# Performance work log

Hardware: AMD Instinct MI355X
Metric: run time of the kernel (lower is better)

Reference implementation:

```python
import jax, jax.numpy as jnp
import numpy as np

N, E, G, ND, H, C, L = 100000, 640000, 1000, 128, 128, 10, 4
ATOMS_PER_GRAPH = 100  # N = G * ATOMS_PER_GRAPH
NEG_SLOPE = 0.01  # nn.LeakyReLU default


def setup_inputs() -> dict:
    key = jax.random.key(0)
    ks = jax.random.split(key, 16)
    s = 0.05
    return {
        "node_attr": jax.random.normal(ks[0], (N, ND), jnp.float32),
        "edge_index": jax.random.randint(ks[1], (2, E), 0, N, jnp.int64),
        "num_atoms": jnp.full((G,), ATOMS_PER_GRAPH, dtype=jnp.int64),
        "enc_W": jax.random.normal(ks[2], (ND, H), jnp.float32) * s,
        "enc_b": jnp.zeros((H,), jnp.float32),
        "gcn_W": jax.random.normal(ks[3], (L, H, H), jnp.float32) * s,
        "gcn_b": jnp.zeros((L, H), jnp.float32),
        "r_W1": jax.random.normal(ks[4], (H, H), jnp.float32) * s,
        "r_b1": jnp.zeros((H,), jnp.float32),
        "r_W2": jax.random.normal(ks[5], (H, H), jnp.float32) * s,
        "r_b2": jnp.zeros((H,), jnp.float32),
        "s_W1": jax.random.normal(ks[6], (H, H), jnp.float32) * s,
        "s_b1": jnp.zeros((H,), jnp.float32),
        "s_W2": jax.random.normal(ks[7], (H, H), jnp.float32) * s,
        "s_b2": jnp.zeros((H,), jnp.float32),
        "fin_W": jax.random.normal(ks[8], (H, C), jnp.float32) * s,
        "fin_b": jnp.zeros((C,), jnp.float32),
    }


def _leaky(x):
    return jnp.where(x > 0, x, NEG_SLOPE * x)


def reference(node_attr, edge_index, num_atoms, enc_W, enc_b, gcn_W, gcn_b,
              r_W1, r_b1, r_W2, r_b2, s_W1, s_b1, s_W2, s_b2, fin_W, fin_b):
    dst, src = edge_index[0], edge_index[1]
    # degree normalization constant across layers: deg(i) = in-edge count, divide by deg+1
    deg = jax.ops.segment_sum(jnp.ones((E,), node_attr.dtype), dst, num_segments=N)
    inv_deg = 1.0 / (deg + 1.0)  # [N]

    x = node_attr @ enc_W + enc_b  # [N, H]
    for l in range(L):
        h = x @ gcn_W[l] + gcn_b[l]
        agg = jax.ops.segment_sum(h[src], dst, num_segments=N)  # scatter_sum over dst
        x = (h + agg) * inv_deg[:, None]

    # GateMLP: ReLuMLP(x) * SigmoidMLP(x)
    r = _leaky(_leaky(x @ r_W1 + r_b1) @ r_W2 + r_b2)
    g = jax.nn.sigmoid(_leaky(x @ s_W1 + s_b1) @ s_W2 + s_b2)
    x = r * g  # [N, H]

    # graph pooling: scatter_mean over graph ids
    graph_mask = jnp.repeat(jnp.arange(G), num_atoms, total_repeat_length=N)
    gsum = jax.ops.segment_sum(x, graph_mask, num_segments=G)
    cnt = jax.ops.segment_sum(jnp.ones((N,), x.dtype), graph_mask, num_segments=G)
    graph_attr = gsum / jnp.maximum(cnt, 1.0)[:, None]  # [G, H]
    return graph_attr @ fin_W + fin_b  # [G, C]
```

## Files before the change

### kernel.cpp

```cpp
#include <hip/hip_runtime.h>
#include <hip/hip_bf16.h>
#include <cstddef>
#include <cstdint>

#define CAP 40
#define LEAK 0.01f

typedef __attribute__((ext_vector_type(8))) short short8v;
typedef __attribute__((ext_vector_type(4))) float float4v;

__device__ __forceinline__ unsigned short f2bf(float f) {
    uint32_t u = __float_as_uint(f);
    uint32_t r = (u + 0x7FFFu + ((u >> 16) & 1u)) >> 16;
    return (unsigned short)r;
}
__device__ __forceinline__ float bf2f(unsigned short s) {
    return __uint_as_float(((uint32_t)s) << 16);
}
__device__ __forceinline__ short8v frag_from_pairs(uint32_t p0, uint32_t p1,
                                                   uint32_t p2, uint32_t p3) {
    union { uint32_t u[4]; short8v v; } c;
    c.u[0] = p0; c.u[1] = p1; c.u[2] = p2; c.u[3] = p3;
    return c.v;
}

__global__ void build_buckets(const int* __restrict__ ei, int E_,
                              int* __restrict__ cnt, int* __restrict__ bucket) {
    int e = (blockIdx.x * 256 + threadIdx.x) * 4;
    if (e >= E_) return;
    if (e + 4 <= E_) {
        int4 d4 = *(const int4*)&ei[e];
        int4 s4 = *(const int4*)&ei[(size_t)E_ + e];
        int p0 = atomicAdd(&cnt[d4.x], 1);
        int p1 = atomicAdd(&cnt[d4.y], 1);
        int p2 = atomicAdd(&cnt[d4.z], 1);
        int p3 = atomicAdd(&cnt[d4.w], 1);
        if (p0 < CAP) bucket[(size_t)d4.x * CAP + p0] = s4.x;
        if (p1 < CAP) bucket[(size_t)d4.y * CAP + p1] = s4.y;
        if (p2 < CAP) bucket[(size_t)d4.z * CAP + p2] = s4.z;
        if (p3 < CAP) bucket[(size_t)d4.w * CAP + p3] = s4.w;
    } else {
        for (; e < E_; ++e) {
            int d = ei[e], s = ei[(size_t)E_ + e];
            int p = atomicAdd(&cnt[d], 1);
            if (p < CAP) bucket[(size_t)d * CAP + p] = s;
        }
    }
}

__global__ void pack_w(const float* __restrict__ enc, const float* __restrict__ gcn,
                       const float* __restrict__ rw1, const float* __restrict__ rw2,
                       const float* __restrict__ sw1, const float* __restrict__ sw2,
                       unsigned short* __restrict__ p) {
    int m = blockIdx.x >> 3;
    int idx = (blockIdx.x & 7) * 256 + threadIdx.x;
    const float* W;
    switch (m) {
        case 0: W = enc; break;
        case 1: case 2: case 3: case 4: W = gcn + (size_t)(m - 1) * 16384; break;
        case 5: W = rw1; break;
        case 6: W = rw2; break;
        case 7: W = sw1; break;
        default: W = sw2; break;
    }
    int n = idx & 127;
    int fg = (idx >> 7) & 3;
    int kc = idx >> 9;
    short8v v;
#pragma unroll
    for (int j = 0; j < 8; ++j)
        v[j] = (short)f2bf(W[(size_t)(kc * 32 + fg * 8 + j) * 128 + n]);
    *(short8v*)(p + (size_t)m * 16384 + (size_t)idx * 8) = v;
}

__device__ __forceinline__ void load_wf(const unsigned short* __restrict__ Wpack,
                                        int w, int fr, int fg, short8v wf[2][4]) {
    const short8v* Wp = (const short8v*)Wpack;
#pragma unroll
    for (int t = 0; t < 2; ++t)
#pragma unroll
        for (int kc = 0; kc < 4; ++kc)
            wf[t][kc] = Wp[(kc * 4 + fg) * 128 + w * 32 + t * 16 + fr];
}

__device__ __forceinline__ void mfma_tile(const unsigned short* As, int fr, int fg,
                                          const short8v wf[2][4], float4v acc[4][2]) {
#pragma unroll
    for (int m = 0; m < 4; ++m) {
        acc[m][0] = (float4v){0.f, 0.f, 0.f, 0.f};
        acc[m][1] = (float4v){0.f, 0.f, 0.f, 0.f};
    }
#pragma unroll
    for (int kc = 0; kc < 4; ++kc) {
        short8v a[4];
#pragma unroll
        for (int m = 0; m < 4; ++m) {
            int row = m * 16 + fr;
            int cb = (kc * 64 + fg * 16) ^ ((row & 7) << 4);
            a[m] = *(const short8v*)((const char*)As + row * 256 + cb);
        }
#pragma unroll
        for (int m = 0; m < 4; ++m) {
            acc[m][0] = __builtin_amdgcn_mfma_f32_16x16x32_bf16(a[m], wf[0][kc], acc[m][0], 0, 0, 0);
            acc[m][1] = __builtin_amdgcn_mfma_f32_16x16x32_bf16(a[m], wf[1][kc], acc[m][1], 0, 0, 0);
        }
    }
}

__global__ __launch_bounds__(256) void gemm_enc(const float* __restrict__ Ain,
                                                const unsigned short* __restrict__ Wpack,
                                                const float* __restrict__ bias,
                                                unsigned short* __restrict__ Cout, int M) {
    __shared__ unsigned short As[64 * 128];
    const int tid = threadIdx.x;
    const int lane = tid & 63;
    const int w = tid >> 6;
    const int row0 = blockIdx.x * 64;
    const int fr = lane & 15;
    const int fg = lane >> 4;

    short8v wf[2][4];
    load_wf(Wpack, w, fr, fg, wf);

    {
        const int r = tid >> 2;
        const int cg = tid & 3;
        const int row = row0 + r;
        char* lbase = (char*)As + r * 256;
        const float* Ap = Ain + (size_t)row * 128 + cg * 32;
#pragma unroll
        for (int i = 0; i < 4; ++i) {
            short8v v = {0, 0, 0, 0, 0, 0, 0, 0};
            if (row < M) {
                float4v p = *(const float4v*)(Ap + i * 8);
                float4v q = *(const float4v*)(Ap + i * 8 + 4);
                v[0] = (short)f2bf(p[0]); v[1] = (short)f2bf(p[1]);
                v[2] = (short)f2bf(p[2]); v[3] = (short)f2bf(p[3]);
                v[4] = (short)f2bf(q[0]); v[5] = (short)f2bf(q[1]);
                v[6] = (short)f2bf(q[2]); v[7] = (short)f2bf(q[3]);
            }
            int cb = (cg * 64 + i * 16) ^ ((r & 7) << 4);
            *(short8v*)(lbase + cb) = v;
        }
    }
    __syncthreads();

    float4v acc[4][2];
    mfma_tile(As, fr, fg, wf, acc);

#pragma unroll
    for (int t = 0; t < 2; ++t) {
        const int col = w * 32 + t * 16 + fr;
        const float bv = bias[col];
#pragma unroll
        for (int m = 0; m < 4; ++m)
#pragma unroll
            for (int q = 0; q < 4; ++q) {
                int row = row0 + m * 16 + fg * 4 + q;
                if (row < M) Cout[(size_t)row * 128 + col] = f2bf(acc[m][t][q] + bv);
            }
    }
}

__device__ __forceinline__ void acc8(float a[8], uint4 v, float m) {
    a[0] = fmaf(m, bf2f((unsigned short)(v.x & 0xffff)), a[0]);
    a[1] = fmaf(m, bf2f((unsigned short)(v.x >> 16)), a[1]);
    a[2] = fmaf(m, bf2f((unsigned short)(v.y & 0xffff)), a[2]);
    a[3] = fmaf(m, bf2f((unsigned short)(v.y >> 16)), a[3]);
    a[4] = fmaf(m, bf2f((unsigned short)(v.z & 0xffff)), a[4]);
    a[5] = fmaf(m, bf2f((unsigned short)(v.z >> 16)), a[5]);
    a[6] = fmaf(m, bf2f((unsigned short)(v.w & 0xffff)), a[6]);
    a[7] = fmaf(m, bf2f((unsigned short)(v.w >> 16)), a[7]);
}

__global__ __launch_bounds__(256, 4) void gcn_fused(const unsigned short* __restrict__ x,
                                                    const int* __restrict__ bucket,
                                                    const int* __restrict__ cnt,
                                                    const unsigned short* __restrict__ Wpack,
                                                    const float* __restrict__ bias,
                                                    unsigned short* __restrict__ xout,
                                                    int Nn) {
    __shared__ unsigned short As[64 * 128];
    const int tid = threadIdx.x;
    const int lane = tid & 63;
    const int w = tid >> 6;
    const int row0 = blockIdx.x * 64;
    const int fr = lane & 15;
    const int fg = lane >> 4;
    const int l16 = lane & 15;
    const int g = lane >> 4;
    const int gl = lane & 48;
    const char* xb = (const char*)x;

    int cfull = 0;
    if (lane < 16) {
        int gn = row0 + w * 16 + lane;
        if (gn >= Nn) gn = Nn - 1;
        cfull = cnt[gn];
    }
    uint4 own[4];
    int2 pre[4];
#pragma unroll
    for (int p = 0; p < 4; ++p) {
        int gn = row0 + w * 16 + p * 4 + g;
        if (gn >= Nn) gn = Nn - 1;
        own[p] = *(const uint4*)(xb + (size_t)gn * 256 + l16 * 16);
        pre[p] = *(const int2*)&bucket[(size_t)gn * CAP + 2 * l16];
    }

#pragma unroll
    for (int p = 0; p < 4; ++p) {
        const int n = p * 4 + g;
        const int r = w * 16 + n;
        const int dfull = __shfl(cfull, n);
        const float id = 1.0f / (float)(dfull + 1);
        const int d = min(dfull, CAP);
        const int dm = min(d, 32);

        float a[8];
        {
            uint4 o = own[p];
            a[0] = bf2f((unsigned short)(o.x & 0xffff));
            a[1] = bf2f((unsigned short)(o.x >> 16));
            a[2] = bf2f((unsigned short)(o.y & 0xffff));
            a[3] = bf2f((unsigned short)(o.y >> 16));
            a[4] = bf2f((unsigned short)(o.z & 0xffff));
            a[5] = bf2f((unsigned short)(o.z >> 16));
            a[6] = bf2f((unsigned short)(o.w & 0xffff));
            a[7] = bf2f((unsigned short)(o.w >> 16));
        }

        for (int j = 0; j < dm; j += 4) {
            int sl = gl + (j >> 1);
            int s0 = __shfl(pre[p].x, sl);
            int s1 = __shfl(pre[p].y, sl);
            int s2 = __shfl(pre[p].x, sl + 1);
            int s3 = __shfl(pre[p].y, sl + 1);
            s0 = min(max(s0, 0), Nn - 1);
            s1 = min(max(s1, 0), Nn - 1);
            s2 = min(max(s2, 0), Nn - 1);
            s3 = min(max(s3, 0), Nn - 1);
            uint4 v0 = *(const uint4*)(xb + (size_t)s0 * 256 + l16 * 16);
            uint4 v1 = *(const uint4*)(xb + (size_t)s1 * 256 + l16 * 16);
            uint4 v2 = *(const uint4*)(xb + (size_t)s2 * 256 + l16 * 16);
            uint4 v3 = *(const uint4*)(xb + (size_t)s3 * 256 + l16 * 16);
            acc8(a, v0, (j + 0 < d) ? 1.f : 0.f);
            acc8(a, v1, (j + 1 < d) ? 1.f : 0.f);
            acc8(a, v2, (j + 2 < d) ? 1.f : 0.f);
            acc8(a, v3, (j + 3 < d) ? 1.f : 0.f);
        }
        if (d > 32) {
            int gn = row0 + r; if (gn >= Nn) gn = Nn - 1;
            for (int j = 32; j < d; ++j) {
                int s = bucket[(size_t)gn * CAP + j];
                uint4 v = *(const uint4*)(xb + (size_t)s * 256 + l16 * 16);
                acc8(a, v, 1.f);
            }
        }

#pragma unroll
        for (int i = 0; i < 8; ++i) a[i] *= id;
        uint4 o;
        o.x = (uint32_t)f2bf(a[0]) | ((uint32_t)f2bf(a[1]) << 16);
        o.y = (uint32_t)f2bf(a[2]) | ((uint32_t)f2bf(a[3]) << 16);
        o.z = (uint32_t)f2bf(a[4]) | ((uint32_t)f2bf(a[5]) << 16);
        o.w = (uint32_t)f2bf(a[6]) | ((uint32_t)f2bf(a[7]) << 16);
        *(uint4*)((char*)As + r * 256 + ((l16 * 16) ^ ((r & 7) << 4))) = o;
    }

    short8v wf[2][4];
    load_wf(Wpack, w, fr, fg, wf);
    __syncthreads();

    float4v acc[4][2];
    mfma_tile(As, fr, fg, wf, acc);

#pragma unroll
    for (int t = 0; t < 2; ++t) {
        const int col = w * 32 + t * 16 + fr;
        const float bv = bias[col];
#pragma unroll
        for (int m = 0; m < 4; ++m)
#pragma unroll
            for (int q = 0; q < 4; ++q) {
                int row = row0 + m * 16 + fg * 4 + q;
                if (row < Nn) xout[(size_t)row * 128 + col] = f2bf(acc[m][t][q] + bv);
            }
    }
}

__global__ __launch_bounds__(256) void gate_fused(const unsigned short* __restrict__ x,
                                                  const unsigned short* __restrict__ wpack,
                                                  const float* __restrict__ rb1,
                                                  const float* __restrict__ rb2,
                                                  const float* __restrict__ sb1,
                                                  const float* __restrict__ sb2,
                                                  unsigned short* __restrict__ out, int M) {
    __shared__ unsigned short Ws[128 * 128];
    const int tid = threadIdx.x;
    const int lane = tid & 63;
    const int w = tid >> 6;
    const int l16 = lane & 15;
    const int fg = lane >> 4;
    const int row0 = blockIdx.x * 64 + w * 16;

    int xr = row0 + l16;
    if (xr >= M) xr = M - 1;
    short8v xbf[4];
#pragma unroll
    for (int kc = 0; kc < 4; ++kc)
        xbf[kc] = *(const short8v*)(x + (size_t)xr * 128 + kc * 32 + fg * 8);

    const short8v* WL = (const short8v*)Ws;
    uint32_t upR[8][2], upS[8][2];

#define STAGE(mi)                                                             \
    {                                                                         \
        const short8v* src = (const short8v*)(wpack + (size_t)(mi) * 16384);  \
        short8v* dst = (short8v*)Ws;                                          \
        _Pragma("unroll") for (int i = 0; i < 8; ++i)                         \
            dst[i * 256 + tid] = src[i * 256 + tid];                          \
    }

#define PASS1(BIAS, UP)                                                       \
    _Pragma("unroll") for (int nt = 0; nt < 8; ++nt) {                        \
        float4v acc = (float4v){0.f, 0.f, 0.f, 0.f};                          \
        _Pragma("unroll") for (int kc = 0; kc < 4; ++kc)                      \
            acc = __builtin_amdgcn_mfma_f32_16x16x32_bf16(                    \
                WL[(kc * 4 + fg) * 128 + nt * 16 + l16], xbf[kc], acc, 0, 0, 0); \
        _Pragma("unroll") for (int q = 0; q < 4; ++q) {                       \
            float v = acc[q] + (BIAS)[nt * 16 + fg * 4 + q];                  \
            acc[q] = v > 0.f ? v : LEAK * v;                                  \
        }                                                                     \
        UP[nt][0] = (uint32_t)f2bf(acc[0]) | ((uint32_t)f2bf(acc[1]) << 16);  \
        UP[nt][1] = (uint32_t)f2bf(acc[2]) | ((uint32_t)f2bf(acc[3]) << 16);  \
    }

#define MKUF(UP, UF)                                                          \
    _Pragma("unroll") for (int kc = 0; kc < 4; ++kc) {                        \
        uint32_t pr0, pr1, pr2, pr3;                                          \
        {                                                                     \
            int srcl = (((2 * fg + 0) & 3) << 4) + l16;                       \
            uint32_t lo = __shfl((int)UP[2 * kc][0], srcl);                   \
            uint32_t hi = __shfl((int)UP[2 * kc + 1][0], srcl);               \
            pr0 = (fg & 2) ? hi : lo;                                         \
            lo = __shfl((int)UP[2 * kc][1], srcl);                            \
            hi = __shfl((int)UP[2 * kc + 1][1], srcl);                        \
            pr1 = (fg & 2) ? hi : lo;                                         \
        }                                                                     \
        {                                                                     \
            int srcl = (((2 * fg + 1) & 3) << 4) + l16;                       \
            uint32_t lo = __shfl((int)UP[2 * kc][0], srcl);                   \
            uint32_t hi = __shfl((int)UP[2 * kc + 1][0], srcl);               \
            pr2 = (fg & 2) ? hi : lo;                                         \
            lo = __shfl((int)UP[2 * kc][1], srcl);                            \
            hi = __shfl((int)UP[2 * kc + 1][1], srcl);                        \
            pr3 = (fg & 2) ? hi : lo;                                         \
        }                                                                     \
        UF[kc] = frag_from_pairs(pr0, pr1, pr2, pr3);                         \
    }

#define PASS2(UF, ACCOUT)                                                     \
    _Pragma("unroll") for (int t2 = 0; t2 < 8; ++t2) {                        \
        float4v acc = (float4v){0.f, 0.f, 0.f, 0.f};                          \
        _Pragma("unroll") for (int kc = 0; kc < 4; ++kc)                      \
            acc = __builtin_amdgcn_mfma_f32_16x16x32_bf16(                    \
                UF[kc], WL[(kc * 4 + fg) * 128 + t2 * 16 + l16], acc, 0, 0, 0); \
        ACCOUT[t2] = acc;                                                     \
    }

    STAGE(5); __syncthreads();
    PASS1(rb1, upR);
    __syncthreads();
    STAGE(7); __syncthreads();
    PASS1(sb1, upS);
    __syncthreads();
    STAGE(6); __syncthreads();
    short8v uf[4];
    MKUF(upR, uf);
    float4v rf[8];
    PASS2(uf, rf);
#pragma unroll
    for (int t2 = 0; t2 < 8; ++t2) {
        float bv = rb2[t2 * 16 + l16];
#pragma unroll
        for (int q = 0; q < 4; ++q) {
            float v = rf[t2][q] + bv;
            rf[t2][q] = v > 0.f ? v : LEAK * v;
        }
    }
    __syncthreads();
    STAGE(8); __syncthreads();
    MKUF(upS, uf);
    float4v gacc[8];
    PASS2(uf, gacc);
#pragma unroll
    for (int t2 = 0; t2 < 8; ++t2) {
        float bv = sb2[t2 * 16 + l16];
#pragma unroll
        for (int q = 0; q < 4; ++q) {
            int row = row0 + fg * 4 + q;
            if (row < M) {
                float gg = 1.f / (1.f + __expf(-(gacc[t2][q] + bv)));
                out[(size_t)row * 128 + t2 * 16 + l16] = f2bf(gg * rf[t2][q]);
            }
        }
    }
#undef STAGE
#undef PASS1
#undef MKUF
#undef PASS2
}

__global__ void scan_atoms(const int* __restrict__ na, int* __restrict__ goff, int G_) {
    __shared__ int sh[1024];
    int t = threadIdx.x;
    int v = (t < G_) ? na[t] : 0;
    sh[t] = v;
    __syncthreads();
    for (int ofs = 1; ofs < 1024; ofs <<= 1) {
        int u = (t >= ofs) ? sh[t - ofs] : 0;
        __syncthreads();
        sh[t] += u;
        __syncthreads();
    }
    if (t == 0) goff[0] = 0;
    if (t < G_) goff[t + 1] = sh[t];
}

__global__ void pool(const unsigned short* __restrict__ x, const int* __restrict__ goff,
                     float* __restrict__ gattr, int G_) {
    int g = blockIdx.x * 2 + (threadIdx.x >> 7);
    if (g >= G_) return;
    int d = threadIdx.x & 127;
    int a0 = goff[g], a1 = goff[g + 1];
    float s0 = 0.f, s1 = 0.f, s2 = 0.f, s3 = 0.f;
    int a = a0;
    for (; a + 4 <= a1; a += 4) {
        s0 += bf2f(x[(size_t)(a + 0) * 128 + d]);
        s1 += bf2f(x[(size_t)(a + 1) * 128 + d]);
        s2 += bf2f(x[(size_t)(a + 2) * 128 + d]);
        s3 += bf2f(x[(size_t)(a + 3) * 128 + d]);
    }
    for (; a < a1; ++a) s0 += bf2f(x[(size_t)a * 128 + d]);
    float s = (s0 + s1) + (s2 + s3);
    float c = (float)max(a1 - a0, 1);
    gattr[(size_t)g * 128 + d] = s / c;
}

__global__ void final_gemm(const float* __restrict__ gattr, const float* __restrict__ fW,
                           const float* __restrict__ fb, float* __restrict__ out,
                           int G_, int C_) {
    int i = blockIdx.x * 256 + threadIdx.x;
    if (i >= G_ * C_) return;
    int g = i / C_, c = i % C_;
    const float* row = gattr + (size_t)g * 128;
    float s = fb[c];
    for (int k = 0; k < 128; ++k) s = fmaf(row[k], fW[k * C_ + c], s);
    out[i] = s;
}

extern "C" void kernel_launch(void* const* d_in, const int* in_sizes, int n_in,
                              void* d_out, int out_size, void* d_ws, size_t ws_size,
                              hipStream_t stream) {
    const float* node_attr = (const float*)d_in[0];
    const int* edge_index  = (const int*)d_in[1];
    const int* num_atoms   = (const int*)d_in[2];
    const float* enc_W = (const float*)d_in[3];
    const float* enc_b = (const float*)d_in[4];
    const float* gcn_W = (const float*)d_in[5];
    const float* gcn_b = (const float*)d_in[6];
    const float* r_W1 = (const float*)d_in[7];
    const float* r_b1 = (const float*)d_in[8];
    const float* r_W2 = (const float*)d_in[9];
    const float* r_b2 = (const float*)d_in[10];
    const float* s_W1 = (const float*)d_in[11];
    const float* s_b1 = (const float*)d_in[12];
    const float* s_W2 = (const float*)d_in[13];
    const float* s_b2 = (const float*)d_in[14];
    const float* fin_W = (const float*)d_in[15];
    const float* fin_b = (const float*)d_in[16];
    float* out = (float*)d_out;

    const int N_ = in_sizes[0] / 128;
    const int E_ = in_sizes[1] / 2;
    const int G_ = in_sizes[2];
    const int C_ = in_sizes[16];

    size_t off = 0;
    auto alloc = [&](size_t bytes) -> void* {
        void* p = (char*)d_ws + off;
        off += (bytes + 255) & ~(size_t)255;
        return p;
    };
    unsigned short* bx = (unsigned short*)alloc((size_t)N_ * 128 * 2);
    unsigned short* bh = (unsigned short*)alloc((size_t)N_ * 128 * 2);
    int* bucket = (int*)alloc((size_t)N_ * CAP * 4);
    int* cnt    = (int*)alloc((size_t)N_ * 4);
    unsigned short* wpack = (unsigned short*)alloc((size_t)9 * 16384 * 2);
    int* goff   = (int*)alloc((size_t)(G_ + 1) * 4);
    float* gattr = (float*)alloc((size_t)G_ * 128 * 4);
    (void)ws_size; (void)n_in; (void)out_size;

    const int gemm_grid = (N_ + 63) / 64;

    hipMemsetAsync(cnt, 0, (size_t)N_ * 4, stream);
    build_buckets<<<(E_ / 4 + 255) / 256, 256, 0, stream>>>(edge_index, E_, cnt, bucket);
    pack_w<<<72, 256, 0, stream>>>(enc_W, gcn_W, r_W1, r_W2, s_W1, s_W2, wpack);
    scan_atoms<<<1, 1024, 0, stream>>>(num_atoms, goff, G_);

    gemm_enc<<<gemm_grid, 256, 0, stream>>>(node_attr, wpack, enc_b, bx, N_);

    unsigned short* cur = bx;
    unsigned short* nxt = bh;
    for (int l = 0; l < 4; ++l) {
        gcn_fused<<<gemm_grid, 256, 0, stream>>>(cur, bucket, cnt,
                                                 wpack + (size_t)(1 + l) * 16384,
                                                 gcn_b + (size_t)l * 128, nxt, N_);
        unsigned short* t = cur; cur = nxt; nxt = t;
    }

    gate_fused<<<gemm_grid, 256, 0, stream>>>(cur, wpack, r_b1, r_b2, s_b1, s_b2, nxt, N_);

    pool<<<(G_ + 1) / 2, 256, 0, stream>>>(nxt, goff, gattr, G_);
    final_gemm<<<(G_ * C_ + 255) / 256, 256, 0, stream>>>(gattr, fin_W, fin_b, out, G_, C_);
}
```

Baseline: 305.1 us.

## Double gate-MLP weight staging and block size to halve barriers and restaging

The gate kernel now uses 512-thread blocks covering 128 rows and stages two 128x128 weight matrices into shared memory at once (r_W1 with s_W1, then r_W2 with s_W2). This cuts the number of staging rounds and block barriers from eight to four and amortizes each weight load over twice as many rows. The second-layer MFMA results now go straight into the bias and activation epilogue, which removes the separate accumulator arrays. In exchange each block uses 64KB of shared memory, which can limit how many blocks fit per CU, and the block count is halved.

```diff
diff --git a/kernel.cpp b/kernel.cpp
--- a/kernel.cpp
+++ b/kernel.cpp
@@ -289,20 +289,20 @@
     }
 }
 
-__global__ __launch_bounds__(256) void gate_fused(const unsigned short* __restrict__ x,
-                                                  const unsigned short* __restrict__ wpack,
-                                                  const float* __restrict__ rb1,
-                                                  const float* __restrict__ rb2,
-                                                  const float* __restrict__ sb1,
-                                                  const float* __restrict__ sb2,
-                                                  unsigned short* __restrict__ out, int M) {
-    __shared__ unsigned short Ws[128 * 128];
+__global__ __launch_bounds__(512, 4) void gate_fused(const unsigned short* __restrict__ x,
+                                                     const unsigned short* __restrict__ wpack,
+                                                     const float* __restrict__ rb1,
+                                                     const float* __restrict__ rb2,
+                                                     const float* __restrict__ sb1,
+                                                     const float* __restrict__ sb2,
+                                                     unsigned short* __restrict__ out, int M) {
+    __shared__ unsigned short Ws[2 * 128 * 128];
     const int tid = threadIdx.x;
     const int lane = tid & 63;
     const int w = tid >> 6;
     const int l16 = lane & 15;
     const int fg = lane >> 4;
-    const int row0 = blockIdx.x * 64 + w * 16;
+    const int row0 = blockIdx.x * 128 + w * 16;
 
     int xr = row0 + l16;
     if (xr >= M) xr = M - 1;
@@ -314,20 +314,23 @@
     const short8v* WL = (const short8v*)Ws;
     uint32_t upR[8][2], upS[8][2];
 
-#define STAGE(mi)                                                             \
+#define STAGE2(mi0, mi1)                                                      \
     {                                                                         \
-        const short8v* src = (const short8v*)(wpack + (size_t)(mi) * 16384);  \
+        const short8v* s0 = (const short8v*)(wpack + (size_t)(mi0) * 16384);  \
+        const short8v* s1 = (const short8v*)(wpack + (size_t)(mi1) * 16384);  \
         short8v* dst = (short8v*)Ws;                                          \
-        _Pragma("unroll") for (int i = 0; i < 8; ++i)                         \
-            dst[i * 256 + tid] = src[i * 256 + tid];                          \
-    }
-
-#define PASS1(BIAS, UP)                                                       \
+        _Pragma("unroll") for (int i = 0; i < 4; ++i)                         \
+            dst[i * 512 + tid] = s0[i * 512 + tid];                           \
+        _Pragma("unroll") for (int i = 0; i < 4; ++i)                         \
+            dst[2048 + i * 512 + tid] = s1[i * 512 + tid];                    \
+    }
+
+#define PASS1(OFS, BIAS, UP)                                                  \
     _Pragma("unroll") for (int nt = 0; nt < 8; ++nt) {                        \
         float4v acc = (float4v){0.f, 0.f, 0.f, 0.f};                          \
         _Pragma("unroll") for (int kc = 0; kc < 4; ++kc)                      \
             acc = __builtin_amdgcn_mfma_f32_16x16x32_bf16(                    \
-                WL[(kc * 4 + fg) * 128 + nt * 16 + l16], xbf[kc], acc, 0, 0, 0); \
+                WL[(OFS) + (kc * 4 + fg) * 128 + nt * 16 + l16], xbf[kc], acc, 0, 0, 0); \
         _Pragma("unroll") for (int q = 0; q < 4; ++q) {                       \
             float v = acc[q] + (BIAS)[nt * 16 + fg * 4 + q];                  \
             acc[q] = v > 0.f ? v : LEAK * v;                                  \
@@ -360,56 +363,54 @@
         UF[kc] = frag_from_pairs(pr0, pr1, pr2, pr3);                         \
     }
 
-#define PASS2(UF, ACCOUT)                                                     \
-    _Pragma("unroll") for (int t2 = 0; t2 < 8; ++t2) {                        \
-        float4v acc = (float4v){0.f, 0.f, 0.f, 0.f};                          \
-        _Pragma("unroll") for (int kc = 0; kc < 4; ++kc)                      \
-            acc = __builtin_amdgcn_mfma_f32_16x16x32_bf16(                    \
-                UF[kc], WL[(kc * 4 + fg) * 128 + t2 * 16 + l16], acc, 0, 0, 0); \
-        ACCOUT[t2] = acc;                                                     \
-    }
-
-    STAGE(5); __syncthreads();
-    PASS1(rb1, upR);
+    STAGE2(5, 7);
     __syncthreads();
-    STAGE(7); __syncthreads();
-    PASS1(sb1, upS);
+    PASS1(0, rb1, upR);
+    PASS1(2048, sb1, upS);
     __syncthreads();
-    STAGE(6); __syncthreads();
+
+    STAGE2(6, 8);
+    __syncthreads();
+
     short8v uf[4];
     MKUF(upR, uf);
     float4v rf[8];
-    PASS2(uf, rf);
 #pragma unroll
     for (int t2 = 0; t2 < 8; ++t2) {
-        float bv = rb2[t2 * 16 + l16];
+        float4v acc = (float4v){0.f, 0.f, 0.f, 0.f};
+#pragma unroll
+        for (int kc = 0; kc < 4; ++kc)
+            acc = __builtin_amdgcn_mfma_f32_16x16x32_bf16(
+                uf[kc], WL[(kc * 4 + fg) * 128 + t2 * 16 + l16], acc, 0, 0, 0);
+        const float bv = rb2[t2 * 16 + l16];
 #pragma unroll
         for (int q = 0; q < 4; ++q) {
-            float v = rf[t2][q] + bv;
+            float v = acc[q] + bv;
             rf[t2][q] = v > 0.f ? v : LEAK * v;
         }
     }
-    __syncthreads();
-    STAGE(8); __syncthreads();
+
     MKUF(upS, uf);
-    float4v gacc[8];
-    PASS2(uf, gacc);
 #pragma unroll
     for (int t2 = 0; t2 < 8; ++t2) {
-        float bv = sb2[t2 * 16 + l16];
+        float4v acc = (float4v){0.f, 0.f, 0.f, 0.f};
+#pragma unroll
+        for (int kc = 0; kc < 4; ++kc)
+            acc = __builtin_amdgcn_mfma_f32_16x16x32_bf16(
+                uf[kc], WL[2048 + (kc * 4 + fg) * 128 + t2 * 16 + l16], acc, 0, 0, 0);
+        const float bv = sb2[t2 * 16 + l16];
 #pragma unroll
         for (int q = 0; q < 4; ++q) {
             int row = row0 + fg * 4 + q;
             if (row < M) {
-                float gg = 1.f / (1.f + __expf(-(gacc[t2][q] + bv)));
+                float gg = 1.f / (1.f + __expf(-(acc[q] + bv)));
                 out[(size_t)row * 128 + t2 * 16 + l16] = f2bf(gg * rf[t2][q]);
             }
         }
     }
-#undef STAGE
+#undef STAGE2
 #undef PASS1
 #undef MKUF
-#undef PASS2
 }
 
 __global__ void scan_atoms(const int* __restrict__ na, int* __restrict__ goff, int G_) {
@@ -520,7 +521,8 @@
         unsigned short* t = cur; cur = nxt; nxt = t;
     }
 
-    gate_fused<<<gemm_grid, 256, 0, stream>>>(cur, wpack, r_b1, r_b2, s_b1, s_b2, nxt, N_);
+    gate_fused<<<(N_ + 127) / 128, 512, 0, stream>>>(cur, wpack, r_b1, r_b2, s_b1, s_b2,
+                                                     nxt, N_);
 
     pool<<<(G_ + 1) / 2, 256, 0, stream>>>(nxt, goff, gattr, G_);
     final_gemm<<<(G_ * C_ + 255) / 256, 256, 0, stream>>>(gattr, fin_W, fin_b, out, G_, C_);
```

Result: faster. 297.5 us (-2.5%).
